# Performance work log

Hardware: AMD Instinct MI355X
Metric: run time of the kernel (lower is better)

## Reference

```python
import jax, jax.numpy as jnp
import numpy as np

BT, N, C, H, W = 1, 4, 64, 28, 60
ZC, YC, XC = 200, 8, 200  # grid dims (Zcam, Ycam, Xcam); voxel_shape=[200,200,8] -> Z=200, X=200, Y=8
OUT_C = 128
EPS = 1e-6


def setup_inputs() -> dict:
    key = jax.random.key(0)
    k1, k2, k3, k4 = jax.random.split(key, 4)
    # normalized sampling coords in ~[-1.2, 1.2] so some points fall outside the image (zero-padded)
    voxcam_coords = jax.random.uniform(k1, (BT, N, ZC, YC, XC, 3), jnp.float32, -1.2, 1.2)
    # binary visibility mask per voxel-camera pair
    vox_valid = (jax.random.uniform(k2, (BT, N, ZC, YC, XC, 1)) < 0.5).astype(jnp.float32)
    img_feats = jax.random.normal(k3, (BT, N, C, H, W), jnp.float32)
    W_comp = jax.random.normal(k4, (OUT_C, C * YC), jnp.float32) * 0.02  # MLP-as-1x1-conv height compressor
    b_comp = jnp.zeros((OUT_C,), jnp.float32)
    return {"voxcam_coords": voxcam_coords, "vox_valid": vox_valid, "img_feats": img_feats,
            "W_comp": W_comp, "b_comp": b_comp}


def _grid_sample_3d(feat, grid):
    """Trilinear grid_sample, align_corners=False, zeros padding.
    feat: (B, C, D, H, W); grid: (B, P, 3) with (x, y, z) in [-1, 1]. Returns (B, C, P)."""
    B, Cc, D, Hh, Ww = feat.shape
    x = ((grid[..., 0] + 1.0) * Ww - 1.0) * 0.5
    y = ((grid[..., 1] + 1.0) * Hh - 1.0) * 0.5
    z = ((grid[..., 2] + 1.0) * D - 1.0) * 0.5
    x0f, y0f, z0f = jnp.floor(x), jnp.floor(y), jnp.floor(z)
    wx, wy, wz = x - x0f, y - y0f, z - z0f
    x0, y0, z0 = x0f.astype(jnp.int32), y0f.astype(jnp.int32), z0f.astype(jnp.int32)

    def sample_one(fb, x0b, y0b, z0b, wxb, wyb, wzb):
        out = jnp.zeros((Cc, x0b.shape[0]), fb.dtype)
        for dz in (0, 1):
            for dy in (0, 1):
                for dx in (0, 1):
                    zi, yi, xi = z0b + dz, y0b + dy, x0b + dx
                    valid = ((zi >= 0) & (zi < D) & (yi >= 0) & (yi < Hh)
                             & (xi >= 0) & (xi < Ww)).astype(fb.dtype)
                    v = fb[:, jnp.clip(zi, 0, D - 1), jnp.clip(yi, 0, Hh - 1), jnp.clip(xi, 0, Ww - 1)]
                    w = ((wxb if dx else 1.0 - wxb) * (wyb if dy else 1.0 - wyb)
                         * (wzb if dz else 1.0 - wzb)) * valid
                    out = out + v * w[None]
        return out

    return jax.vmap(sample_one)(feat, x0, y0, z0, wx, wy, wz)


def reference(voxcam_coords, vox_valid, img_feats, W_comp, b_comp):
    bt, n, zc, yc, xc, _ = voxcam_coords.shape
    c, h, w = img_feats.shape[2], img_feats.shape[3], img_feats.shape[4]
    P = zc * yc * xc
    grid = voxcam_coords.reshape(bt * n, P, 3)
    feat = img_feats.reshape(bt * n, c, 1, h, w)  # N_group=1 depth axis
    sampled = _grid_sample_3d(feat, grid).reshape(bt, n, c, zc, yc, xc)
    mask = jnp.transpose(vox_valid, (0, 1, 5, 2, 3, 4))  # (bt, n, 1, zc, yc, xc)
    vox_feats = sampled * mask                      # get_feats_dense_grid_sample masking
    # reduce_cams: masked mean over cameras (dim=1)
    red = (vox_feats * mask).sum(axis=1) / (mask.sum(axis=1) + EPS)  # (bt, c, zc, yc, xc)
    # height compressor: 'bt c z y x -> bt (c y) z x' then 1x1 conv (MLP)
    comp_in = jnp.transpose(red, (0, 1, 3, 2, 4)).reshape(bt, c * yc, zc, xc)
    out = jnp.einsum('bczx,oc->bozx', comp_in, W_comp) + b_comp[None, :, None, None]
    # _unpack_batch: (b*t, C, Z, X) -> (b, t, C, Z, X) with b=t=1
    return out.reshape(1, bt, out.shape[1], zc, xc)
```

## Files before the change

kernel.cpp:

```cpp
#include <hip/hip_runtime.h>
#include <hip/hip_bf16.h>
#include <hip/hip_fp16.h>

#define N_  4
#define C_  64
#define H_  28
#define W_  60
#define ZC_ 200
#define YC_ 8
#define XC_ 200
#define OUTC_ 128
#define KD_ 512
#define EPS_ 1e-6f
#define ZB 4
#define XB 8
#define NCOL 32

typedef __attribute__((ext_vector_type(8))) short short8;
typedef __attribute__((ext_vector_type(4))) float f32x4;

__device__ __forceinline__ unsigned short f2bf(float f) {
    unsigned int u = __float_as_uint(f);
    u += 0x7FFF + ((u >> 16) & 1);
    return (unsigned short)(u >> 16);
}

__global__ void gsvt_prep(const float* __restrict__ img,
                          const float* __restrict__ Wc,
                          unsigned short* __restrict__ featB,
                          unsigned short* __restrict__ Wb) {
    int tid = blockIdx.x * blockDim.x + threadIdx.x;
    int stride = gridDim.x * blockDim.x;
    const int totF = N_ * H_ * W_ * C_;
    for (int i = tid; i < totF; i += stride) {
        int c  = i & 63;
        int hw = i >> 6;
        int w  = hw % W_;
        int nh = hw / W_;
        int h  = nh % H_;
        int n  = nh / H_;
        featB[i] = f2bf(img[((n * C_ + c) * H_ + h) * W_ + w]);
    }
    const int totW = OUTC_ * KD_;
    for (int i = tid; i < totW; i += stride) {
        int k = i & (KD_ - 1);
        int o = i >> 9;
        int y = k >> 6;
        int c = k & 63;
        Wb[i] = f2bf(Wc[o * KD_ + c * YC_ + y]);
    }
}

__device__ __forceinline__ void accp(float2* n, const uint4 V, const float w) {
    float2 f0, f1, f2, f3;
    f0.x = __uint_as_float(V.x << 16); f0.y = __uint_as_float(V.x & 0xFFFF0000u);
    f1.x = __uint_as_float(V.y << 16); f1.y = __uint_as_float(V.y & 0xFFFF0000u);
    f2.x = __uint_as_float(V.z << 16); f2.y = __uint_as_float(V.z & 0xFFFF0000u);
    f3.x = __uint_as_float(V.w << 16); f3.y = __uint_as_float(V.w & 0xFFFF0000u);
    n[0].x += w * f0.x; n[0].y += w * f0.y;
    n[1].x += w * f1.x; n[1].y += w * f1.y;
    n[2].x += w * f2.x; n[2].y += w * f2.y;
    n[3].x += w * f3.x; n[3].y += w * f3.y;
}

__global__ __launch_bounds__(256, 4) void gsvt_fused2(
        const float* __restrict__ coords,
        const float* __restrict__ validm,
        const unsigned short* __restrict__ featB,
        const unsigned short* __restrict__ Wb,
        const float* __restrict__ bias,
        float* __restrict__ out)
{
    __shared__ uint2 tab2[N_ * 256];
    __shared__ unsigned short redB[64][NCOL][8];
    float (*ms)[4] = (float(*)[4])&redB[0][0][0];
    unsigned* cmaskA = (unsigned*)((char*)&redB[0][0][0] + 4096);

    const int z0 = blockIdx.y * ZB;
    const int x0 = blockIdx.x * XB;
    const int t  = threadIdx.x;

    const int p0   = t;
    const int y0_  = t >> 5;
    const int col0 = t & 31;
    const int zg   = z0 + (col0 >> 3);
    const int xg   = x0 + (col0 & 7);

    if (t < NCOL) cmaskA[t] = 0u;

    float gx[4], gy[4], gzv[4], mm[4];
    #pragma unroll
    for (int cam = 0; cam < N_; ++cam) {
        const int cb = ((cam * ZC_ + zg) * YC_ + y0_) * XC_ + xg;
        gx[cam]  = coords[cb * 3 + 0];
        gy[cam]  = coords[cb * 3 + 1];
        gzv[cam] = coords[cb * 3 + 2];
        mm[cam]  = validm[cb];
        ms[p0][cam] = mm[cam];
    }
    __syncthreads();

    {
        const float inv = 1.0f / (ms[p0][0] + ms[p0][1] + ms[p0][2] + ms[p0][3] + EPS_);
        #pragma unroll
        for (int cam = 0; cam < N_; ++cam) {
            const float xf = ((gx[cam] + 1.0f) * (float)W_ - 1.0f) * 0.5f;
            const float yf = ((gy[cam] + 1.0f) * (float)H_ - 1.0f) * 0.5f;
            const float zf = gzv[cam] * 0.5f;
            const float x0f = floorf(xf), y0f = floorf(yf), z0f = floorf(zf);
            const float wx = xf - x0f, wy = yf - y0f, wz = zf - z0f;
            const int xi = (int)x0f, yi = (int)y0f, zi = (int)z0f;

            const float zw = (zi == 0) ? (1.f - wz) : ((zi == -1) ? wz : 0.f);
            const float s  = mm[cam] * zw * inv;

            const float wx0 = (xi >= 0 && xi < W_)         ? (1.f - wx) * s : 0.f;
            const float wx1 = (xi + 1 >= 0 && xi + 1 < W_) ? wx * s         : 0.f;
            const float wy0 = (yi >= 0 && yi < H_)         ? (1.f - wy)     : 0.f;
            const float wy1 = (yi + 1 >= 0 && yi + 1 < H_) ? wy             : 0.f;

            const unsigned q00 = (unsigned)(wy0 * wx0 * 4095.f + 0.5f);
            const unsigned q01 = (unsigned)(wy0 * wx1 * 4095.f + 0.5f);
            const unsigned q10 = (unsigned)(wy1 * wx0 * 4095.f + 0.5f);
            const unsigned q11 = (unsigned)(wy1 * wx1 * 4095.f + 0.5f);

            const int xc0 = min(max(xi, 0), W_ - 1);
            const int xc1 = min(max(xi + 1, 0), W_ - 1);
            const int yc0 = min(max(yi, 0), H_ - 1);
            const int yc1 = min(max(yi + 1, 0), H_ - 1);
            const unsigned pixidx = (unsigned)((cam * H_ + yc0) * W_ + xc0);
            const unsigned fdx = (unsigned)(xc1 - xc0);
            const unsigned fdy = (unsigned)(yc1 - yc0);

            const unsigned A = q00 | (q01 << 12) | ((q10 & 0xFFu) << 24);
            const unsigned B = (q10 >> 8) | (q11 << 4) | (pixidx << 16)
                             | (fdx << 29) | (fdy << 30);
            tab2[cam * 256 + p0] = make_uint2(A, B);

            if (q00 | q01 | q10 | q11)
                atomicOr(&cmaskA[col0], 1u << (y0_ * 4 + cam));
        }
    }
    __syncthreads();

    const int grp   = t >> 3;
    const int lane8 = t & 7;
    const unsigned cm = cmaskA[grp];
    __syncthreads();

    const unsigned lb = (unsigned)(lane8 << 4);
    const char* fb = (const char*)featB;

    #pragma unroll
    for (int y = 0; y < YC_; ++y) {
        const int p    = y * 32 + grp;
        const int kb   = y * 8 + lane8;
        const int pcol = (grp & 16) | ((grp ^ kb) & 15);

        unsigned sub = (cm >> (y * 4)) & 0xFu;
        uint4 R = make_uint4(0u, 0u, 0u, 0u);

        if (sub) {
            float2 num[4] = {{0.f,0.f},{0.f,0.f},{0.f,0.f},{0.f,0.f}};
            while (sub) {
                const int cam = __builtin_ctz(sub);
                sub &= sub - 1u;
                const uint2 T = tab2[cam * 256 + p];
                const float w00 = (float)(T.x & 0xFFFu)                      * (1.f/4095.f);
                const float w01 = (float)((T.x >> 12) & 0xFFFu)              * (1.f/4095.f);
                const float w10 = (float)((T.x >> 24) | ((T.y & 0xFu) << 8)) * (1.f/4095.f);
                const float w11 = (float)((T.y >> 4) & 0xFFFu)               * (1.f/4095.f);
                const unsigned base = (((T.y >> 16) & 0x1FFFu) << 7) + lb;
                const unsigned dxo  = ((T.y >> 29) & 1u) << 7;
                const unsigned dyo  = ((T.y >> 30) & 1u) * (unsigned)(W_ * 128);
                const uint4 V0 = *(const uint4*)(fb + base);
                const uint4 V1 = *(const uint4*)(fb + (base + dxo));
                const uint4 V2 = *(const uint4*)(fb + (base + dyo));
                const uint4 V3 = *(const uint4*)(fb + (base + dyo + dxo));
                accp(num, V0, w00);
                accp(num, V1, w01);
                accp(num, V2, w10);
                accp(num, V3, w11);
            }
            unsigned r0, r1, r2, r3;
            asm("v_cvt_pk_bf16_f32 %0, %1, %2" : "=v"(r0) : "v"(num[0].x), "v"(num[0].y));
            asm("v_cvt_pk_bf16_f32 %0, %1, %2" : "=v"(r1) : "v"(num[1].x), "v"(num[1].y));
            asm("v_cvt_pk_bf16_f32 %0, %1, %2" : "=v"(r2) : "v"(num[2].x), "v"(num[2].y));
            asm("v_cvt_pk_bf16_f32 %0, %1, %2" : "=v"(r3) : "v"(num[3].x), "v"(num[3].y));
            R = make_uint4(r0, r1, r2, r3);
        }
        *(uint4*)&redB[kb][pcol][0] = R;
    }
    __syncthreads();

    const int wave = t >> 6;
    const int lane = t & 63;
    const int q    = lane >> 4;
    const int l16  = lane & 15;

    f32x4 acc00 = {0.f,0.f,0.f,0.f}, acc01 = {0.f,0.f,0.f,0.f};
    f32x4 acc10 = {0.f,0.f,0.f,0.f}, acc11 = {0.f,0.f,0.f,0.f};
    const unsigned short* wbase = Wb + (wave * 32 + l16) * KD_;

    #pragma unroll
    for (int ks = 0; ks < 16; ++ks) {
        const int kb = ks * 4 + q;
        const int xs = l16 ^ (kb & 15);
        const short8 B0 = *(const short8*)&redB[kb][xs][0];
        const short8 B1 = *(const short8*)&redB[kb][16 + xs][0];
        const short8 A0 = *(const short8*)(wbase + ks * 32 + q * 8);
        const short8 A1 = *(const short8*)(wbase + 16 * KD_ + ks * 32 + q * 8);
        acc00 = __builtin_amdgcn_mfma_f32_16x16x32_bf16(A0, B0, acc00, 0, 0, 0);
        acc01 = __builtin_amdgcn_mfma_f32_16x16x32_bf16(A0, B1, acc01, 0, 0, 0);
        acc10 = __builtin_amdgcn_mfma_f32_16x16x32_bf16(A1, B0, acc10, 0, 0, 0);
        acc11 = __builtin_amdgcn_mfma_f32_16x16x32_bf16(A1, B1, acc11, 0, 0, 0);
    }

    #pragma unroll
    for (int ct = 0; ct < 2; ++ct) {
        const int col = ct * 16 + l16;
        const int zz  = col >> 3;
        const int xl  = col & 7;
        const int ob  = (z0 + zz) * XC_ + x0 + xl;
        const f32x4 a0 = ct ? acc01 : acc00;
        const f32x4 a1 = ct ? acc11 : acc10;
        #pragma unroll
        for (int j = 0; j < 4; ++j) {
            const int o0 = wave * 32 + q * 4 + j;
            out[o0 * (ZC_ * XC_) + ob] = a0[j] + bias[o0];
            const int o1 = o0 + 16;
            out[o1 * (ZC_ * XC_) + ob] = a1[j] + bias[o1];
        }
    }
}

extern "C" void kernel_launch(void* const* d_in, const int* in_sizes, int n_in,
                              void* d_out, int out_size, void* d_ws, size_t ws_size,
                              hipStream_t stream) {
    const float* coords = (const float*)d_in[0];
    const float* validm = (const float*)d_in[1];
    const float* img    = (const float*)d_in[2];
    const float* Wc     = (const float*)d_in[3];
    const float* bias   = (const float*)d_in[4];
    float* out = (float*)d_out;

    unsigned short* featB = (unsigned short*)d_ws;
    unsigned short* Wb    = featB + (N_ * H_ * W_ * C_);

    gsvt_prep<<<512, 256, 0, stream>>>(img, Wc, featB, Wb);

    dim3 grid(XC_ / XB, ZC_ / ZB);
    gsvt_fused2<<<grid, 256, 0, stream>>>(coords, validm, featB, Wb, bias, out);
}
```

Measured before the change: 56.12 us.

## Halve block tile to 16 columns and split cameras and heights across threads

Each block now covers 2 z rows instead of 4, giving 16 output columns per block, so the grid doubles to 1250 blocks. Inside a block the thread mapping changes: coordinate loading splits the cameras between two thread halves, and each sampling group handles 4 heights instead of 8. This shortens per-thread serial work and raises the launch-bounds occupancy target. In exchange, every wave reloads the same W_comp tiles for half as many columns, so weight traffic per output doubles, and the MFMA stage has half the reuse per block.

```diff
diff --git a/kernel.cpp b/kernel.cpp
--- a/kernel.cpp
+++ b/kernel.cpp
@@ -12,9 +12,9 @@
 #define OUTC_ 128
 #define KD_ 512
 #define EPS_ 1e-6f
-#define ZB 4
+#define ZB 2
 #define XB 8
-#define NCOL 32
+#define NCOL 16
 
 typedef __attribute__((ext_vector_type(8))) short short8;
 typedef __attribute__((ext_vector_type(4))) float f32x4;
@@ -63,7 +63,7 @@
     n[3].x += w * f3.x; n[3].y += w * f3.y;
 }
 
-__global__ __launch_bounds__(256, 4) void gsvt_fused2(
+__global__ __launch_bounds__(256, 8) void gsvt_fused16(
         const float* __restrict__ coords,
         const float* __restrict__ validm,
         const unsigned short* __restrict__ featB,
@@ -71,48 +71,51 @@
         const float* __restrict__ bias,
         float* __restrict__ out)
 {
-    __shared__ uint2 tab2[N_ * 256];
+    __shared__ uint2 tab2[N_ * 128];
     __shared__ unsigned short redB[64][NCOL][8];
     float (*ms)[4] = (float(*)[4])&redB[0][0][0];
-    unsigned* cmaskA = (unsigned*)((char*)&redB[0][0][0] + 4096);
+    unsigned* cmaskA = (unsigned*)((char*)&redB[0][0][0] + 2048);
 
     const int z0 = blockIdx.y * ZB;
     const int x0 = blockIdx.x * XB;
     const int t  = threadIdx.x;
 
-    const int p0   = t;
-    const int y0_  = t >> 5;
-    const int col0 = t & 31;
+    const int p0   = t & 127;
+    const int y0_  = p0 >> 4;
+    const int col0 = p0 & 15;
     const int zg   = z0 + (col0 >> 3);
     const int xg   = x0 + (col0 & 7);
+    const int cam0 = (t >> 7) * 2;
 
     if (t < NCOL) cmaskA[t] = 0u;
 
-    float gx[4], gy[4], gzv[4], mm[4];
-    #pragma unroll
-    for (int cam = 0; cam < N_; ++cam) {
+    float gx[2], gy[2], gzv[2], mm[2];
+    #pragma unroll
+    for (int ii = 0; ii < 2; ++ii) {
+        const int cam = cam0 + ii;
         const int cb = ((cam * ZC_ + zg) * YC_ + y0_) * XC_ + xg;
-        gx[cam]  = coords[cb * 3 + 0];
-        gy[cam]  = coords[cb * 3 + 1];
-        gzv[cam] = coords[cb * 3 + 2];
-        mm[cam]  = validm[cb];
-        ms[p0][cam] = mm[cam];
+        gx[ii]  = coords[cb * 3 + 0];
+        gy[ii]  = coords[cb * 3 + 1];
+        gzv[ii] = coords[cb * 3 + 2];
+        mm[ii]  = validm[cb];
+        ms[p0][cam] = mm[ii];
     }
     __syncthreads();
 
     {
         const float inv = 1.0f / (ms[p0][0] + ms[p0][1] + ms[p0][2] + ms[p0][3] + EPS_);
         #pragma unroll
-        for (int cam = 0; cam < N_; ++cam) {
-            const float xf = ((gx[cam] + 1.0f) * (float)W_ - 1.0f) * 0.5f;
-            const float yf = ((gy[cam] + 1.0f) * (float)H_ - 1.0f) * 0.5f;
-            const float zf = gzv[cam] * 0.5f;
+        for (int ii = 0; ii < 2; ++ii) {
+            const int cam = cam0 + ii;
+            const float xf = ((gx[ii] + 1.0f) * (float)W_ - 1.0f) * 0.5f;
+            const float yf = ((gy[ii] + 1.0f) * (float)H_ - 1.0f) * 0.5f;
+            const float zf = gzv[ii] * 0.5f;
             const float x0f = floorf(xf), y0f = floorf(yf), z0f = floorf(zf);
             const float wx = xf - x0f, wy = yf - y0f, wz = zf - z0f;
             const int xi = (int)x0f, yi = (int)y0f, zi = (int)z0f;
 
             const float zw = (zi == 0) ? (1.f - wz) : ((zi == -1) ? wz : 0.f);
-            const float s  = mm[cam] * zw * inv;
+            const float s  = mm[ii] * zw * inv;
 
             const float wx0 = (xi >= 0 && xi < W_)         ? (1.f - wx) * s : 0.f;
             const float wx1 = (xi + 1 >= 0 && xi + 1 < W_) ? wx * s         : 0.f;
@@ -135,7 +138,7 @@
             const unsigned A = q00 | (q01 << 12) | ((q10 & 0xFFu) << 24);
             const unsigned B = (q10 >> 8) | (q11 << 4) | (pixidx << 16)
                              | (fdx << 29) | (fdy << 30);
-            tab2[cam * 256 + p0] = make_uint2(A, B);
+            tab2[cam * 128 + p0] = make_uint2(A, B);
 
             if (q00 | q01 | q10 | q11)
                 atomicOr(&cmaskA[col0], 1u << (y0_ * 4 + cam));
@@ -145,17 +148,20 @@
 
     const int grp   = t >> 3;
     const int lane8 = t & 7;
-    const unsigned cm = cmaskA[grp];
+    const int col   = grp & 15;
+    const int ybase = (grp >> 4) * 4;
+    const unsigned cm = cmaskA[col];
     __syncthreads();
 
     const unsigned lb = (unsigned)(lane8 << 4);
     const char* fb = (const char*)featB;
 
     #pragma unroll
-    for (int y = 0; y < YC_; ++y) {
-        const int p    = y * 32 + grp;
+    for (int i = 0; i < 4; ++i) {
+        const int y    = ybase + i;
+        const int p    = y * 16 + col;
         const int kb   = y * 8 + lane8;
-        const int pcol = (grp & 16) | ((grp ^ kb) & 15);
+        const int pcol = col ^ (kb & 15);
 
         unsigned sub = (cm >> (y * 4)) & 0xFu;
         uint4 R = make_uint4(0u, 0u, 0u, 0u);
@@ -165,7 +171,7 @@
             while (sub) {
                 const int cam = __builtin_ctz(sub);
                 sub &= sub - 1u;
-                const uint2 T = tab2[cam * 256 + p];
+                const uint2 T = tab2[cam * 128 + p];
                 const float w00 = (float)(T.x & 0xFFFu)                      * (1.f/4095.f);
                 const float w01 = (float)((T.x >> 12) & 0xFFFu)              * (1.f/4095.f);
                 const float w10 = (float)((T.x >> 24) | ((T.y & 0xFu) << 8)) * (1.f/4095.f);
@@ -198,39 +204,27 @@
     const int q    = lane >> 4;
     const int l16  = lane & 15;
 
-    f32x4 acc00 = {0.f,0.f,0.f,0.f}, acc01 = {0.f,0.f,0.f,0.f};
-    f32x4 acc10 = {0.f,0.f,0.f,0.f}, acc11 = {0.f,0.f,0.f,0.f};
+    f32x4 acc0 = {0.f,0.f,0.f,0.f}, acc1 = {0.f,0.f,0.f,0.f};
     const unsigned short* wbase = Wb + (wave * 32 + l16) * KD_;
 
     #pragma unroll
     for (int ks = 0; ks < 16; ++ks) {
         const int kb = ks * 4 + q;
         const int xs = l16 ^ (kb & 15);
-        const short8 B0 = *(const short8*)&redB[kb][xs][0];
-        const short8 B1 = *(const short8*)&redB[kb][16 + xs][0];
+        const short8 Bf = *(const short8*)&redB[kb][xs][0];
         const short8 A0 = *(const short8*)(wbase + ks * 32 + q * 8);
         const short8 A1 = *(const short8*)(wbase + 16 * KD_ + ks * 32 + q * 8);
-        acc00 = __builtin_amdgcn_mfma_f32_16x16x32_bf16(A0, B0, acc00, 0, 0, 0);
-        acc01 = __builtin_amdgcn_mfma_f32_16x16x32_bf16(A0, B1, acc01, 0, 0, 0);
-        acc10 = __builtin_amdgcn_mfma_f32_16x16x32_bf16(A1, B0, acc10, 0, 0, 0);
-        acc11 = __builtin_amdgcn_mfma_f32_16x16x32_bf16(A1, B1, acc11, 0, 0, 0);
-    }
-
-    #pragma unroll
-    for (int ct = 0; ct < 2; ++ct) {
-        const int col = ct * 16 + l16;
-        const int zz  = col >> 3;
-        const int xl  = col & 7;
-        const int ob  = (z0 + zz) * XC_ + x0 + xl;
-        const f32x4 a0 = ct ? acc01 : acc00;
-        const f32x4 a1 = ct ? acc11 : acc10;
-        #pragma unroll
-        for (int j = 0; j < 4; ++j) {
-            const int o0 = wave * 32 + q * 4 + j;
-            out[o0 * (ZC_ * XC_) + ob] = a0[j] + bias[o0];
-            const int o1 = o0 + 16;
-            out[o1 * (ZC_ * XC_) + ob] = a1[j] + bias[o1];
-        }
+        acc0 = __builtin_amdgcn_mfma_f32_16x16x32_bf16(A0, Bf, acc0, 0, 0, 0);
+        acc1 = __builtin_amdgcn_mfma_f32_16x16x32_bf16(A1, Bf, acc1, 0, 0, 0);
+    }
+
+    const int ob = (z0 + (l16 >> 3)) * XC_ + x0 + (l16 & 7);
+    #pragma unroll
+    for (int j = 0; j < 4; ++j) {
+        const int o0 = wave * 32 + q * 4 + j;
+        out[o0 * (ZC_ * XC_) + ob] = acc0[j] + bias[o0];
+        const int o1 = o0 + 16;
+        out[o1 * (ZC_ * XC_) + ob] = acc1[j] + bias[o1];
     }
 }
 
@@ -250,5 +244,5 @@
     gsvt_prep<<<512, 256, 0, stream>>>(img, Wc, featB, Wb);
 
     dim3 grid(XC_ / XB, ZC_ / ZB);
-    gsvt_fused2<<<grid, 256, 0, stream>>>(coords, validm, featB, Wb, bias, out);
-}
+    gsvt_fused16<<<grid, 256, 0, stream>>>(coords, validm, featB, Wb, bias, out);
+}
```

Result: slower. 70.48 us (+25.6%).

## Issue all camera feature loads up front with manual vmcnt waits, drop sparsity mask

Applied to the files above, without the earlier changes.

Replaces the per-group sparse camera loop, which relied on an atomic-built mask and a data-dependent while loop, with a branch-free sequence. All 16 bf16 feature loads for the four cameras are issued together through inline asm, and explicit s_waitcnt plus sched_barrier stages the accumulation per camera. Inactive cameras load from a harmless in-bounds base address with zero weights. This is meant to raise memory-level parallelism and remove the atomics, the divergence and one barrier. In exchange it always performs the loads, even for masked cameras, uses more registers, and lowers the launch-bounds occupancy hint from 4 to 3.

```diff
diff --git a/kernel.cpp b/kernel.cpp
--- a/kernel.cpp
+++ b/kernel.cpp
@@ -18,6 +18,7 @@
 
 typedef __attribute__((ext_vector_type(8))) short short8;
 typedef __attribute__((ext_vector_type(4))) float f32x4;
+typedef __attribute__((ext_vector_type(4))) unsigned int u32x4;
 
 __device__ __forceinline__ unsigned short f2bf(float f) {
     unsigned int u = __float_as_uint(f);
@@ -51,7 +52,7 @@
     }
 }
 
-__device__ __forceinline__ void accp(float2* n, const uint4 V, const float w) {
+__device__ __forceinline__ void accp(float2* n, const u32x4 V, const float w) {
     float2 f0, f1, f2, f3;
     f0.x = __uint_as_float(V.x << 16); f0.y = __uint_as_float(V.x & 0xFFFF0000u);
     f1.x = __uint_as_float(V.y << 16); f1.y = __uint_as_float(V.y & 0xFFFF0000u);
@@ -63,7 +64,7 @@
     n[3].x += w * f3.x; n[3].y += w * f3.y;
 }
 
-__global__ __launch_bounds__(256, 4) void gsvt_fused2(
+__global__ __launch_bounds__(256, 3) void gsvt_fusedA(
         const float* __restrict__ coords,
         const float* __restrict__ validm,
         const unsigned short* __restrict__ featB,
@@ -74,7 +75,6 @@
     __shared__ uint2 tab2[N_ * 256];
     __shared__ unsigned short redB[64][NCOL][8];
     float (*ms)[4] = (float(*)[4])&redB[0][0][0];
-    unsigned* cmaskA = (unsigned*)((char*)&redB[0][0][0] + 4096);
 
     const int z0 = blockIdx.y * ZB;
     const int x0 = blockIdx.x * XB;
@@ -85,8 +85,6 @@
     const int col0 = t & 31;
     const int zg   = z0 + (col0 >> 3);
     const int xg   = x0 + (col0 & 7);
-
-    if (t < NCOL) cmaskA[t] = 0u;
 
     float gx[4], gy[4], gzv[4], mm[4];
     #pragma unroll
@@ -136,61 +134,78 @@
             const unsigned B = (q10 >> 8) | (q11 << 4) | (pixidx << 16)
                              | (fdx << 29) | (fdy << 30);
             tab2[cam * 256 + p0] = make_uint2(A, B);
-
-            if (q00 | q01 | q10 | q11)
-                atomicOr(&cmaskA[col0], 1u << (y0_ * 4 + cam));
         }
     }
     __syncthreads();
 
     const int grp   = t >> 3;
     const int lane8 = t & 7;
-    const unsigned cm = cmaskA[grp];
-    __syncthreads();
-
     const unsigned lb = (unsigned)(lane8 << 4);
     const char* fb = (const char*)featB;
 
+    #define ISSUE(V, A_) asm volatile("global_load_dwordx4 %0, %1, off" \
+                                      : "=v"(V) : "v"(A_))
+    #define WAITV(n) do { asm volatile("s_waitcnt vmcnt(" #n ")"); \
+                          __builtin_amdgcn_sched_barrier(0); } while (0)
+
     #pragma unroll
     for (int y = 0; y < YC_; ++y) {
-        const int p    = y * 32 + grp;
+        const int p = y * 32 + grp;
+
+        const uint2 T0 = tab2[0 * 256 + p];
+        const uint2 T1 = tab2[1 * 256 + p];
+        const uint2 T2 = tab2[2 * 256 + p];
+        const uint2 T3 = tab2[3 * 256 + p];
+
+        u32x4 V00, V01, V02, V03, V10, V11, V12, V13;
+        u32x4 V20, V21, V22, V23, V30, V31, V32, V33;
+        #define ADDR_ISSUE(Tv, Va, Vb, Vc, Vd)                                 \
+            {                                                                  \
+                const bool act = (Tv.x | (Tv.y & 0xFFFFu)) != 0u;              \
+                const unsigned base = act ? ((((Tv.y >> 16) & 0x1FFFu) << 7) + lb) : lb; \
+                const unsigned dxo  = act ? (((Tv.y >> 29) & 1u) << 7) : 0u;   \
+                const unsigned dyo  = act ? (((Tv.y >> 30) & 1u) * (unsigned)(W_ * 128)) : 0u; \
+                ISSUE(Va, fb + base);                                          \
+                ISSUE(Vb, fb + (base + dxo));                                  \
+                ISSUE(Vc, fb + (base + dyo));                                  \
+                ISSUE(Vd, fb + (base + dyo + dxo));                            \
+            }
+        ADDR_ISSUE(T0, V00, V01, V02, V03)
+        ADDR_ISSUE(T1, V10, V11, V12, V13)
+        ADDR_ISSUE(T2, V20, V21, V22, V23)
+        ADDR_ISSUE(T3, V30, V31, V32, V33)
+        #undef ADDR_ISSUE
+
+        float2 num[4] = {{0.f,0.f},{0.f,0.f},{0.f,0.f},{0.f,0.f}};
+
+        #define DECW(Tv, w00, w01, w10, w11)                                   \
+            const float w00 = (float)(Tv.x & 0xFFFu)                        * (1.f/4095.f); \
+            const float w01 = (float)((Tv.x >> 12) & 0xFFFu)                * (1.f/4095.f); \
+            const float w10 = (float)((Tv.x >> 24) | ((Tv.y & 0xFu) << 8)) * (1.f/4095.f); \
+            const float w11 = (float)((Tv.y >> 4) & 0xFFFu)                 * (1.f/4095.f);
+
+        { DECW(T0, a, b, c, d) WAITV(12);
+          accp(num, V00, a); accp(num, V01, b); accp(num, V02, c); accp(num, V03, d); }
+        { DECW(T1, a, b, c, d) WAITV(8);
+          accp(num, V10, a); accp(num, V11, b); accp(num, V12, c); accp(num, V13, d); }
+        { DECW(T2, a, b, c, d) WAITV(4);
+          accp(num, V20, a); accp(num, V21, b); accp(num, V22, c); accp(num, V23, d); }
+        { DECW(T3, a, b, c, d) WAITV(0);
+          accp(num, V30, a); accp(num, V31, b); accp(num, V32, c); accp(num, V33, d); }
+        #undef DECW
+
+        unsigned r0, r1, r2, r3;
+        asm("v_cvt_pk_bf16_f32 %0, %1, %2" : "=v"(r0) : "v"(num[0].x), "v"(num[0].y));
+        asm("v_cvt_pk_bf16_f32 %0, %1, %2" : "=v"(r1) : "v"(num[1].x), "v"(num[1].y));
+        asm("v_cvt_pk_bf16_f32 %0, %1, %2" : "=v"(r2) : "v"(num[2].x), "v"(num[2].y));
+        asm("v_cvt_pk_bf16_f32 %0, %1, %2" : "=v"(r3) : "v"(num[3].x), "v"(num[3].y));
+
         const int kb   = y * 8 + lane8;
         const int pcol = (grp & 16) | ((grp ^ kb) & 15);
-
-        unsigned sub = (cm >> (y * 4)) & 0xFu;
-        uint4 R = make_uint4(0u, 0u, 0u, 0u);
-
-        if (sub) {
-            float2 num[4] = {{0.f,0.f},{0.f,0.f},{0.f,0.f},{0.f,0.f}};
-            while (sub) {
-                const int cam = __builtin_ctz(sub);
-                sub &= sub - 1u;
-                const uint2 T = tab2[cam * 256 + p];
-                const float w00 = (float)(T.x & 0xFFFu)                      * (1.f/4095.f);
-                const float w01 = (float)((T.x >> 12) & 0xFFFu)              * (1.f/4095.f);
-                const float w10 = (float)((T.x >> 24) | ((T.y & 0xFu) << 8)) * (1.f/4095.f);
-                const float w11 = (float)((T.y >> 4) & 0xFFFu)               * (1.f/4095.f);
-                const unsigned base = (((T.y >> 16) & 0x1FFFu) << 7) + lb;
-                const unsigned dxo  = ((T.y >> 29) & 1u) << 7;
-                const unsigned dyo  = ((T.y >> 30) & 1u) * (unsigned)(W_ * 128);
-                const uint4 V0 = *(const uint4*)(fb + base);
-                const uint4 V1 = *(const uint4*)(fb + (base + dxo));
-                const uint4 V2 = *(const uint4*)(fb + (base + dyo));
-                const uint4 V3 = *(const uint4*)(fb + (base + dyo + dxo));
-                accp(num, V0, w00);
-                accp(num, V1, w01);
-                accp(num, V2, w10);
-                accp(num, V3, w11);
-            }
-            unsigned r0, r1, r2, r3;
-            asm("v_cvt_pk_bf16_f32 %0, %1, %2" : "=v"(r0) : "v"(num[0].x), "v"(num[0].y));
-            asm("v_cvt_pk_bf16_f32 %0, %1, %2" : "=v"(r1) : "v"(num[1].x), "v"(num[1].y));
-            asm("v_cvt_pk_bf16_f32 %0, %1, %2" : "=v"(r2) : "v"(num[2].x), "v"(num[2].y));
-            asm("v_cvt_pk_bf16_f32 %0, %1, %2" : "=v"(r3) : "v"(num[3].x), "v"(num[3].y));
-            R = make_uint4(r0, r1, r2, r3);
-        }
-        *(uint4*)&redB[kb][pcol][0] = R;
-    }
+        *(uint4*)&redB[kb][pcol][0] = make_uint4(r0, r1, r2, r3);
+    }
+    #undef ISSUE
+    #undef WAITV
     __syncthreads();
 
     const int wave = t >> 6;
@@ -218,9 +233,9 @@
 
     #pragma unroll
     for (int ct = 0; ct < 2; ++ct) {
-        const int col = ct * 16 + l16;
-        const int zz  = col >> 3;
-        const int xl  = col & 7;
+        const int c2  = ct * 16 + l16;
+        const int zz  = c2 >> 3;
+        const int xl  = c2 & 7;
         const int ob  = (z0 + zz) * XC_ + x0 + xl;
         const f32x4 a0 = ct ? acc01 : acc00;
         const f32x4 a1 = ct ? acc11 : acc10;
@@ -250,5 +265,5 @@
     gsvt_prep<<<512, 256, 0, stream>>>(img, Wc, featB, Wb);
 
     dim3 grid(XC_ / XB, ZC_ / ZB);
-    gsvt_fused2<<<grid, 256, 0, stream>>>(coords, validm, featB, Wb, bias, out);
-}
+    gsvt_fusedA<<<grid, 256, 0, stream>>>(coords, validm, featB, Wb, bias, out);
+}
```

Result: no change. 56.43 us (+0.5%).
